# Optimization experiments

Measured on AMD Instinct MI355X. Metric: run time of the kernel, lower is better.

Reference implementation:

```python
import jax, jax.numpy as jnp
import numpy as np

N, K, DN, DA, H = 20000, 16, 128, 128, 256
D_IN = DN + DA  # 256


def _lin_init(key, out_dim, in_dim):
    scale = 1.0 / np.sqrt(in_dim)
    return jax.random.uniform(key, (out_dim, in_dim), jnp.float32, -scale, scale)


def setup_inputs() -> dict:
    key = jax.random.key(0)
    ks = jax.random.split(key, 16)
    # adjacency: col 0 = parent index; cols 1..K = neighbor indices, -1 padded.
    parent = jax.random.randint(ks[0], (N, 1), 0, N, dtype=jnp.int32)
    nbr_first = jax.random.randint(ks[1], (N, 1), 0, N, dtype=jnp.int32)  # guarantee >=1 nbr
    nbr_rest = jax.random.randint(ks[2], (N, K - 1), -1, N, dtype=jnp.int32)
    adj = jnp.concatenate([parent, nbr_first, nbr_rest], axis=1)
    names = jax.random.normal(ks[3], (N, DN), jnp.float32)
    attrs = jax.random.normal(ks[4], (N, DA), jnp.float32)
    return {
        "nodeAdjacencySpecTensor": adj,
        "nodeNamesEncoded": names,
        "nodeAttributesEncoded": attrs,
        "W_in": _lin_init(ks[5], H, D_IN),
        "b_in": jnp.zeros((H,), jnp.float32),
        "W_parent": _lin_init(ks[6], H, H),
        "b_parent": jnp.zeros((H,), jnp.float32),
        "W_neighbor": _lin_init(ks[7], H, H),
        "b_neighbor": jnp.zeros((H,), jnp.float32),
        "W_ih": _lin_init(ks[8], 3 * H, H),
        "b_ih": jnp.zeros((3 * H,), jnp.float32),
        "W_hh": _lin_init(ks[9], 3 * H, H),
        "b_hh": jnp.zeros((3 * H,), jnp.float32),
        "depth": 3,
    }


def _gru_cell(x, h, W_ih, b_ih, W_hh, b_hh):
    # torch.nn.GRUCell math; gate order r, z, n.
    gi = x @ W_ih.T + b_ih
    gh = h @ W_hh.T + b_hh
    i_r, i_z, i_n = jnp.split(gi, 3, axis=-1)
    h_r, h_z, h_n = jnp.split(gh, 3, axis=-1)
    r = jax.nn.sigmoid(i_r + h_r)
    z = jax.nn.sigmoid(i_z + h_z)
    n = jnp.tanh(i_n + r * h_n)
    return (1.0 - z) * n + z * h


def reference(nodeAdjacencySpecTensor, nodeNamesEncoded, nodeAttributesEncoded,
              W_in, b_in, W_parent, b_parent, W_neighbor, b_neighbor,
              W_ih, b_ih, W_hh, b_hh, depth):
    adj = nodeAdjacencySpecTensor
    parent_idx = adj[:, 0]                 # [N]
    nbr_idx = adj[:, 1:]                   # [N, K], -1 padded
    mask = (nbr_idx >= 0)                  # [N, K]
    safe_nbr = jnp.clip(nbr_idx, 0, None)
    nbr_count = jnp.maximum(mask.sum(axis=1), 1).astype(jnp.float32)  # [N]

    node_info = jnp.concatenate([nodeNamesEncoded, nodeAttributesEncoded], axis=-1)
    x = node_info @ W_in.T + b_in          # [N, H]

    for _ in range(depth):
        p = x @ W_parent.T + b_parent      # [N, H]
        nbr = x @ W_neighbor.T + b_neighbor  # [N, H]
        # irregular gathers
        parent_feat = p[parent_idx]        # [N, H]
        gathered = nbr[safe_nbr]           # [N, K, H]
        nbr_sum = jnp.sum(gathered * mask[:, :, None], axis=1)  # [N, H]
        summary = parent_feat + nbr_sum / nbr_count[:, None]
        x = _gru_cell(x, summary, W_ih, b_ih, W_hh, b_hh)
    return x
```

## Files before the change

### kernel.cpp

```cpp
#include <hip/hip_runtime.h>
#include <hip/hip_bf16.h>

typedef __bf16 bf16x8 __attribute__((ext_vector_type(8)));
typedef __bf16 bf16x4 __attribute__((ext_vector_type(4)));
typedef float  f32x4  __attribute__((ext_vector_type(4)));

#define NN   20000
#define NADJ 17

__device__ __forceinline__ void xcd_remap(int b, int nwg, int col_shift, int& r, int& c)
{
    int q = nwg >> 3, rem = nwg & 7;
    int x = b & 7, k = b >> 3;
    int start = x * q + (x < rem ? x : rem);
    int idx = start + k;
    r = idx >> col_shift;
    c = idx & ((1 << col_shift) - 1);
}

__global__ void pack_weights_kernel(const float* __restrict__ Win, const float* __restrict__ bin,
                                    const float* __restrict__ Wp,  const float* __restrict__ bp,
                                    const float* __restrict__ Wn,  const float* __restrict__ bn,
                                    const float* __restrict__ Wih, const float* __restrict__ bih,
                                    const float* __restrict__ Whh, const float* __restrict__ bhh,
                                    __bf16* __restrict__ Wb, float* __restrict__ bc)
{
    int idx = blockIdx.x * 256 + threadIdx.x;
    if (idx < 1536) {
        int c = idx; float v;
        if (c < 256)      v = bin[c];
        else if (c < 512) { int j = c - 256; v = bp[j] + bn[j]; }
        else {
            int rel = c - 512;
            int j = (rel >> 6) * 16 + (rel & 15);
            int g = (rel >> 4) & 3;
            if      (g == 0) v = bih[j] + bhh[j];
            else if (g == 1) v = bih[256 + j] + bhh[256 + j];
            else if (g == 2) v = bih[512 + j];
            else             v = bhh[512 + j];
        }
        bc[c] = v;
    }
    if (idx >= 180224) return;
    int e = idx << 2;
    const float* src = nullptr;
    bool zero = false;
    if (e < 65536) {
        int row = e >> 8, k = e & 255;
        src = Win + (size_t)row * 256 + k;
    } else if (e < 196608) {
        int rel = e - 65536;
        int row = rel >> 9, k = rel & 511;
        src = (k < 256) ? (Wp + (size_t)row * 256 + k)
                        : (Wn + (size_t)row * 256 + (k - 256));
    } else {
        int rel = e - 196608;
        int row = rel >> 9, k = rel & 511;
        int j = (row >> 6) * 16 + (row & 15);
        int g = (row >> 4) & 3;
        if (k < 256) {
            if (g == 3) zero = true;
            else {
                int off = (g == 0) ? 0 : (g == 1) ? 256 : 512;
                src = Wih + (size_t)(off + j) * 256 + k;
            }
        } else {
            int k2 = k - 256;
            if (g == 2) zero = true;
            else {
                int off = (g == 0) ? 0 : (g == 1) ? 256 : 512;
                src = Whh + (size_t)(off + j) * 256 + k2;
            }
        }
    }
    float4 v = zero ? make_float4(0.f, 0.f, 0.f, 0.f) : *(const float4*)src;
    bf16x4 o = { (__bf16)v.x, (__bf16)v.y, (__bf16)v.z, (__bf16)v.w };
    *(bf16x4*)(Wb + (size_t)e) = o;
}

__global__ void pack_info_kernel(const float* __restrict__ names, const float* __restrict__ attrs,
                                 __bf16* __restrict__ xb)
{
    int idx = blockIdx.x * 256 + threadIdx.x;
    if (idx >= NN * 64) return;
    int i  = idx >> 6;
    int d4 = (idx & 63) << 2;
    const float* src = (d4 < 128) ? (names + (size_t)i * 128 + d4)
                                  : (attrs + (size_t)i * 128 + (d4 - 128));
    float4 v = *(const float4*)src;
    bf16x4 o = { (__bf16)v.x, (__bf16)v.y, (__bf16)v.z, (__bf16)v.w };
    *(bf16x4*)(xb + (size_t)i * 256 + d4) = o;
}

__global__ void gather_avg_kernel(const int* __restrict__ adj, const __bf16* __restrict__ x,
                                  __bf16* __restrict__ G2)
{
    const int node = blockIdx.x * 4 + (threadIdx.x >> 6);
    const int l = threadIdx.x & 63;
    int av = (l < NADJ) ? adj[(size_t)node * NADJ + l] : -1;
    float s0 = 0.f, s1 = 0.f, s2 = 0.f, s3 = 0.f;
    int cnt = 0;
#pragma unroll
    for (int j = 1; j < NADJ; ++j) {
        int idx = __shfl(av, j, 64);
        if (idx >= 0) {
            ++cnt;
            bf16x4 v = *(const bf16x4*)(x + (size_t)idx * 256 + l * 4);
            s0 += (float)v[0]; s1 += (float)v[1]; s2 += (float)v[2]; s3 += (float)v[3];
        }
    }
    float inv = 1.f / (float)(cnt < 1 ? 1 : cnt);
    bf16x4 o = { (__bf16)(s0 * inv), (__bf16)(s1 * inv), (__bf16)(s2 * inv), (__bf16)(s3 * inv) };
    *(bf16x4*)(G2 + (size_t)node * 256 + l * 4) = o;
}

__global__ __launch_bounds__(256, 4)
void gemm_bias_kernel(const __bf16* __restrict__ A0, const __bf16* __restrict__ A1, int lda,
                      const int* __restrict__ parents, int par_stride,
                      const __bf16* __restrict__ W, int ldw,
                      const float* __restrict__ bias,
                      __bf16* __restrict__ Cb, __bf16* __restrict__ Cl,
                      int n_rows, int n_cols, int kt_n, int nwg, int col_shift)
{
    __shared__ __align__(16) __bf16 As[128 * 64];
    __shared__ __align__(16) __bf16 Bs[128 * 64];
    __shared__ int par_s[128];
    const int t = threadIdx.x;
    const int w = t >> 6;
    const int l = t & 63;
    int rb, cb_;
    xcd_remap(blockIdx.x, nwg, col_shift, rb, cb_);
    const int brow = rb * 128;
    const int bcol = cb_ * 128;
    const int wr = (w >> 1) * 64, wc = (w & 1) * 64;

    if (parents) {
        if (t < 128) {
            int node = brow + t; if (node > n_rows - 1) node = n_rows - 1;
            par_s[t] = parents[(size_t)node * par_stride];
        }
        __syncthreads();
    }

    f32x4 acc[4][4] = {};

    for (int kt = 0; kt < kt_n; ++kt) {
        const int k0 = kt * 64;
#pragma unroll
        for (int i = 0; i < 4; ++i) {
            int f   = i * 256 + t;
            int row = f >> 3;
            int cs  = ((f & 7) * 16) ^ ((row & 7) << 4);
            int ar  = brow + row; if (ar > n_rows - 1) ar = n_rows - 1;
            const __bf16* abase;
            if (parents && k0 < 256)             abase = A0 + (size_t)par_s[row] * 256 + k0;
            else if (A1 != nullptr && k0 >= 256) abase = A1 + (size_t)ar * 256 + (k0 - 256);
            else                                 abase = A0 + (size_t)ar * lda + k0;
            const __bf16* ga = abase + (cs >> 1);
            const __bf16* gb = W + (size_t)(bcol + row) * ldw + k0 + (cs >> 1);
            char* la = (char*)As + (i * 256 + w * 64) * 16;
            char* lb = (char*)Bs + (i * 256 + w * 64) * 16;
            __builtin_amdgcn_global_load_lds(
                (const __attribute__((address_space(1))) unsigned int*)ga,
                (__attribute__((address_space(3))) unsigned int*)la, 16, 0, 0);
            __builtin_amdgcn_global_load_lds(
                (const __attribute__((address_space(1))) unsigned int*)gb,
                (__attribute__((address_space(3))) unsigned int*)lb, 16, 0, 0);
        }
        asm volatile("s_waitcnt vmcnt(0)" ::: "memory");
        __syncthreads();
#pragma unroll
        for (int ks = 0; ks < 2; ++ks) {
            bf16x8 af[4], bfv[4];
#pragma unroll
            for (int m = 0; m < 4; ++m) {
                int row = wr + m * 16 + (l & 15);
                int cb  = (ks * 64 + ((l >> 4) * 16)) ^ ((row & 7) << 4);
                af[m] = *(const bf16x8*)((const char*)As + row * 128 + cb);
            }
#pragma unroll
            for (int n = 0; n < 4; ++n) {
                int row = wc + n * 16 + (l & 15);
                int cb  = (ks * 64 + ((l >> 4) * 16)) ^ ((row & 7) << 4);
                bfv[n] = *(const bf16x8*)((const char*)Bs + row * 128 + cb);
            }
#pragma unroll
            for (int m = 0; m < 4; ++m)
#pragma unroll
                for (int n = 0; n < 4; ++n)
                    acc[m][n] = __builtin_amdgcn_mfma_f32_16x16x32_bf16(af[m], bfv[n], acc[m][n], 0, 0, 0);
        }
        __syncthreads();
    }
#pragma unroll
    for (int m = 0; m < 4; ++m) {
        int r0 = brow + wr + m * 16 + ((l >> 4) * 4);
#pragma unroll
        for (int n = 0; n < 4; ++n) {
            int c = bcol + wc + n * 16 + (l & 15);
            float bv = bias[c];
#pragma unroll
            for (int i = 0; i < 4; ++i) {
                int r = r0 + i;
                if (r < n_rows) {
                    float v = acc[m][n][i] + bv;
                    __bf16 hi = (__bf16)v;
                    Cb[(size_t)r * n_cols + c] = hi;
                    if (Cl) Cl[(size_t)r * n_cols + c] = (__bf16)(v - (float)hi);
                }
            }
        }
    }
}

#define GRU_KT_BODY(K0, ABASE, SKIP_N)                                                  \
    {                                                                                   \
        _Pragma("unroll")                                                               \
        for (int i = 0; i < 4; ++i) {                                                   \
            int f   = i * 256 + t;                                                      \
            int row = f >> 3;                                                           \
            int cs  = ((f & 7) * 16) ^ ((row & 7) << 4);                                \
            int ar  = brow + row; if (ar > n_rows - 1) ar = n_rows - 1;                 \
            const __bf16* ga = (ABASE) + (size_t)ar * 256 + (cs >> 1);                  \
            const __bf16* gb = W + (size_t)(bcol + row) * 512 + (K0) + (cs >> 1);       \
            char* la = (char*)As + (i * 256 + w * 64) * 16;                             \
            char* lb = (char*)Bs + (i * 256 + w * 64) * 16;                             \
            __builtin_amdgcn_global_load_lds(                                           \
                (const __attribute__((address_space(1))) unsigned int*)ga,              \
                (__attribute__((address_space(3))) unsigned int*)la, 16, 0, 0);         \
            if (((row >> 4) & 3) != (SKIP_N))                                           \
                __builtin_amdgcn_global_load_lds(                                       \
                    (const __attribute__((address_space(1))) unsigned int*)gb,          \
                    (__attribute__((address_space(3))) unsigned int*)lb, 16, 0, 0);     \
        }                                                                               \
        asm volatile("s_waitcnt vmcnt(0)" ::: "memory");                                \
        __syncthreads();                                                                \
        _Pragma("unroll")                                                               \
        for (int ks = 0; ks < 2; ++ks) {                                                \
            bf16x8 af[4], bfv[4];                                                       \
            _Pragma("unroll")                                                           \
            for (int m = 0; m < 4; ++m) {                                               \
                int row = wr + m * 16 + (l & 15);                                       \
                int cb  = (ks * 64 + ((l >> 4) * 16)) ^ ((row & 7) << 4);               \
                af[m] = *(const bf16x8*)((const char*)As + row * 128 + cb);             \
            }                                                                           \
            _Pragma("unroll")                                                           \
            for (int n = 0; n < 4; ++n) {                                               \
                if (n == (SKIP_N)) continue;                                            \
                int row = wc + n * 16 + (l & 15);                                       \
                int cb  = (ks * 64 + ((l >> 4) * 16)) ^ ((row & 7) << 4);               \
                bfv[n] = *(const bf16x8*)((const char*)Bs + row * 128 + cb);            \
            }                                                                           \
            _Pragma("unroll")                                                           \
            for (int m = 0; m < 4; ++m)                                                 \
                _Pragma("unroll")                                                       \
                for (int n = 0; n < 4; ++n)                                             \
                    if (n != (SKIP_N))                                                  \
                        acc[m][n] = __builtin_amdgcn_mfma_f32_16x16x32_bf16(            \
                            af[m], bfv[n], acc[m][n], 0, 0, 0);                         \
        }                                                                               \
        __syncthreads();                                                                \
    }

__global__ __launch_bounds__(256, 4)
void gru_gemm_kernel(const __bf16* __restrict__ A0, const __bf16* __restrict__ A1,
                     const __bf16* __restrict__ W,
                     const float* __restrict__ bias,
                     const __bf16* __restrict__ sbh, const __bf16* __restrict__ sbl,
                     float* __restrict__ X, __bf16* __restrict__ xb_next,
                     int n_rows)
{
    __shared__ __align__(16) __bf16 As[128 * 64];
    __shared__ __align__(16) __bf16 Bs[128 * 64];
    const int t = threadIdx.x;
    const int w = t >> 6;
    const int l = t & 63;
    int rb, cb_;
    xcd_remap(blockIdx.x, 157 * 8, 3, rb, cb_);
    const int brow = rb * 128;
    const int bcol = cb_ * 128;
    const int wr = (w >> 1) * 64, wc = (w & 1) * 64;

    f32x4 acc[4][4] = {};

    for (int kt = 0; kt < 4; ++kt) {
        const int k0 = kt * 64;
        GRU_KT_BODY(k0, A0 + k0, 3)
    }
    for (int kt = 4; kt < 8; ++kt) {
        const int k0 = kt * 64;
        GRU_KT_BODY(k0, A1 + (k0 - 256), 2)
    }

    const int jb = ((bcol + wc) >> 6) * 16 + (l & 15);
    const int c0 = bcol + wc + (l & 15);
    const float b0 = bias[c0], b1 = bias[c0 + 16], b2 = bias[c0 + 32], b3 = bias[c0 + 48];
#pragma unroll
    for (int m = 0; m < 4; ++m) {
        int r0 = brow + wr + m * 16 + ((l >> 4) * 4);
#pragma unroll
        for (int i = 0; i < 4; ++i) {
            int r = r0 + i;
            if (r < n_rows) {
                float gr  = acc[m][0][i] + b0;
                float gz  = acc[m][1][i] + b1;
                float gin = acc[m][2][i] + b2;
                float ghn = acc[m][3][i] + b3;
                float rg = 1.f / (1.f + __expf(-gr));
                float zg = 1.f / (1.f + __expf(-gz));
                float a2 = gin + rg * ghn;
                float tt = __expf(-2.f * fabsf(a2));
                float ng = (1.f - tt) / (1.f + tt);
                ng = (a2 < 0.f) ? -ng : ng;
                float h = (float)sbh[(size_t)r * 256 + jb] + (float)sbl[(size_t)r * 256 + jb];
                float out = (1.f - zg) * ng + zg * h;
                if (X)       X[(size_t)r * 256 + jb] = out;
                if (xb_next) xb_next[(size_t)r * 256 + jb] = (__bf16)out;
            }
        }
    }
}

extern "C" void kernel_launch(void* const* d_in, const int* in_sizes, int n_in,
                              void* d_out, int out_size, void* d_ws, size_t ws_size,
                              hipStream_t stream)
{
    const int*   adj   = (const int*)  d_in[0];
    const float* names = (const float*)d_in[1];
    const float* attrs = (const float*)d_in[2];
    const float* Win = (const float*)d_in[3];
    const float* bin = (const float*)d_in[4];
    const float* Wp  = (const float*)d_in[5];
    const float* bp  = (const float*)d_in[6];
    const float* Wn  = (const float*)d_in[7];
    const float* bn  = (const float*)d_in[8];
    const float* Wih = (const float*)d_in[9];
    const float* bih = (const float*)d_in[10];
    const float* Whh = (const float*)d_in[11];
    const float* bhh = (const float*)d_in[12];
    float* X = (float*)d_out;

    char* w = (char*)d_ws;
    __bf16* xinfo = (__bf16*)(w);
    __bf16* xb0   = (__bf16*)(w + 10240000);
    __bf16* xb1   = (__bf16*)(w + 20480000);
    __bf16* sbh   = (__bf16*)(w + 30720000);
    __bf16* sbl   = (__bf16*)(w + 40960000);
    __bf16* G2    = (__bf16*)(w + 51200000);
    __bf16* Wb    = (__bf16*)(w + 61440000);
    float*  bc    = (float*) (w + 62881792);

    pack_weights_kernel<<<704, 256, 0, stream>>>(Win, bin, Wp, bp, Wn, bn, Wih, bih, Whh, bhh, Wb, bc);
    pack_info_kernel<<<5000, 256, 0, stream>>>(names, attrs, xinfo);

    gemm_bias_kernel<<<314, 256, 0, stream>>>(xinfo, nullptr, 256, nullptr, 0,
                                              Wb, 256, bc, xb0, nullptr, NN, 256, 4, 314, 1);

    __bf16* cur = xb0;
    __bf16* nxt = xb1;
    for (int d = 0; d < 3; ++d) {
        gather_avg_kernel<<<5000, 256, 0, stream>>>(adj, cur, G2);
        gemm_bias_kernel<<<314, 256, 0, stream>>>(cur, G2, 256, adj, NADJ,
                                                  Wb + 65536, 512, bc + 256,
                                                  sbh, sbl, NN, 256, 8, 314, 1);
        gru_gemm_kernel<<<1256, 256, 0, stream>>>(cur, sbh, Wb + 196608, bc + 512,
                                                  sbh, sbl, (d == 2) ? X : nullptr,
                                                  (d < 2) ? nxt : nullptr, NN);
        __bf16* tmp = cur; cur = nxt; nxt = tmp;
    }
}
```

Baseline: 259.0 us.

## Double-buffer LDS tiles to overlap global loads with MFMA in both GEMMs

Both the bias GEMM and the GRU GEMM now keep two LDS buffers for the A and B tiles. The loads for the next K tile are issued before the MFMAs run on the current one, and there is one barrier per iteration instead of two. The aim is to hide global-to-LDS load latency behind compute. In exchange, LDS use per block doubles and launch bounds drop from 4 to 2 blocks per CU. The explicit vmcnt(0) wait is removed, so visibility of the async LDS loads now depends on the wait the compiler emits at __syncthreads.

Result: slower. 281.8 us (+8.8%).

```diff
diff --git a/kernel.cpp b/kernel.cpp
--- a/kernel.cpp
+++ b/kernel.cpp
@@ -114,7 +114,7 @@
     *(bf16x4*)(G2 + (size_t)node * 256 + l * 4) = o;
 }
 
-__global__ __launch_bounds__(256, 4)
+__global__ __launch_bounds__(256, 2)
 void gemm_bias_kernel(const __bf16* __restrict__ A0, const __bf16* __restrict__ A1, int lda,
                       const int* __restrict__ parents, int par_stride,
                       const __bf16* __restrict__ W, int ldw,
@@ -122,8 +122,8 @@
                       __bf16* __restrict__ Cb, __bf16* __restrict__ Cl,
                       int n_rows, int n_cols, int kt_n, int nwg, int col_shift)
 {
-    __shared__ __align__(16) __bf16 As[128 * 64];
-    __shared__ __align__(16) __bf16 Bs[128 * 64];
+    __shared__ __align__(16) __bf16 As[2][128 * 64];
+    __shared__ __align__(16) __bf16 Bs[2][128 * 64];
     __shared__ int par_s[128];
     const int t = threadIdx.x;
     const int w = t >> 6;
@@ -142,9 +142,7 @@
         __syncthreads();
     }
 
-    f32x4 acc[4][4] = {};
-
-    for (int kt = 0; kt < kt_n; ++kt) {
+    auto stage = [&](int kt, int buf) {
         const int k0 = kt * 64;
 #pragma unroll
         for (int i = 0; i < 4; ++i) {
@@ -158,8 +156,8 @@
             else                                 abase = A0 + (size_t)ar * lda + k0;
             const __bf16* ga = abase + (cs >> 1);
             const __bf16* gb = W + (size_t)(bcol + row) * ldw + k0 + (cs >> 1);
-            char* la = (char*)As + (i * 256 + w * 64) * 16;
-            char* lb = (char*)Bs + (i * 256 + w * 64) * 16;
+            char* la = (char*)As[buf] + (i * 256 + w * 64) * 16;
+            char* lb = (char*)Bs[buf] + (i * 256 + w * 64) * 16;
             __builtin_amdgcn_global_load_lds(
                 (const __attribute__((address_space(1))) unsigned int*)ga,
                 (__attribute__((address_space(3))) unsigned int*)la, 16, 0, 0);
@@ -167,8 +165,15 @@
                 (const __attribute__((address_space(1))) unsigned int*)gb,
                 (__attribute__((address_space(3))) unsigned int*)lb, 16, 0, 0);
         }
-        asm volatile("s_waitcnt vmcnt(0)" ::: "memory");
-        __syncthreads();
+    };
+
+    f32x4 acc[4][4] = {};
+    stage(0, 0);
+    __syncthreads();
+
+    for (int kt = 0; kt < kt_n; ++kt) {
+        const int buf = kt & 1;
+        if (kt + 1 < kt_n) stage(kt + 1, buf ^ 1);
 #pragma unroll
         for (int ks = 0; ks < 2; ++ks) {
             bf16x8 af[4], bfv[4];
@@ -176,13 +181,13 @@
             for (int m = 0; m < 4; ++m) {
                 int row = wr + m * 16 + (l & 15);
                 int cb  = (ks * 64 + ((l >> 4) * 16)) ^ ((row & 7) << 4);
-                af[m] = *(const bf16x8*)((const char*)As + row * 128 + cb);
+                af[m] = *(const bf16x8*)((const char*)As[buf] + row * 128 + cb);
             }
 #pragma unroll
             for (int n = 0; n < 4; ++n) {
                 int row = wc + n * 16 + (l & 15);
                 int cb  = (ks * 64 + ((l >> 4) * 16)) ^ ((row & 7) << 4);
-                bfv[n] = *(const bf16x8*)((const char*)Bs + row * 128 + cb);
+                bfv[n] = *(const bf16x8*)((const char*)Bs[buf] + row * 128 + cb);
             }
 #pragma unroll
             for (int m = 0; m < 4; ++m)
@@ -190,7 +195,7 @@
                 for (int n = 0; n < 4; ++n)
                     acc[m][n] = __builtin_amdgcn_mfma_f32_16x16x32_bf16(af[m], bfv[n], acc[m][n], 0, 0, 0);
         }
-        __syncthreads();
+        if (kt + 1 < kt_n) __syncthreads();
     }
 #pragma unroll
     for (int m = 0; m < 4; ++m) {
@@ -213,28 +218,33 @@
     }
 }
 
-#define GRU_KT_BODY(K0, ABASE, SKIP_N)                                                  \
+#define GRU_STAGE(KN, BUF)                                                              \
     {                                                                                   \
+        const int k0_   = (KN) * 64;                                                    \
+        const int skip_ = ((KN) < 4) ? 3 : 2;                                           \
+        const __bf16* ab_ = ((KN) < 4) ? (A0 + k0_) : (A1 + (k0_ - 256));               \
         _Pragma("unroll")                                                               \
         for (int i = 0; i < 4; ++i) {                                                   \
             int f   = i * 256 + t;                                                      \
             int row = f >> 3;                                                           \
             int cs  = ((f & 7) * 16) ^ ((row & 7) << 4);                                \
             int ar  = brow + row; if (ar > n_rows - 1) ar = n_rows - 1;                 \
-            const __bf16* ga = (ABASE) + (size_t)ar * 256 + (cs >> 1);                  \
-            const __bf16* gb = W + (size_t)(bcol + row) * 512 + (K0) + (cs >> 1);       \
-            char* la = (char*)As + (i * 256 + w * 64) * 16;                             \
-            char* lb = (char*)Bs + (i * 256 + w * 64) * 16;                             \
+            const __bf16* ga = ab_ + (size_t)ar * 256 + (cs >> 1);                      \
+            const __bf16* gb = W + (size_t)(bcol + row) * 512 + k0_ + (cs >> 1);        \
+            char* la = (char*)As[BUF] + (i * 256 + w * 64) * 16;                        \
+            char* lb = (char*)Bs[BUF] + (i * 256 + w * 64) * 16;                        \
             __builtin_amdgcn_global_load_lds(                                           \
                 (const __attribute__((address_space(1))) unsigned int*)ga,              \
                 (__attribute__((address_space(3))) unsigned int*)la, 16, 0, 0);         \
-            if (((row >> 4) & 3) != (SKIP_N))                                           \
+            if (((row >> 4) & 3) != skip_)                                              \
                 __builtin_amdgcn_global_load_lds(                                       \
                     (const __attribute__((address_space(1))) unsigned int*)gb,          \
                     (__attribute__((address_space(3))) unsigned int*)lb, 16, 0, 0);     \
         }                                                                               \
-        asm volatile("s_waitcnt vmcnt(0)" ::: "memory");                                \
-        __syncthreads();                                                                \
+    }
+
+#define GRU_COMPUTE(BUF, SKIPN)                                                         \
+    {                                                                                   \
         _Pragma("unroll")                                                               \
         for (int ks = 0; ks < 2; ++ks) {                                                \
             bf16x8 af[4], bfv[4];                                                       \
@@ -242,27 +252,26 @@
             for (int m = 0; m < 4; ++m) {                                               \
                 int row = wr + m * 16 + (l & 15);                                       \
                 int cb  = (ks * 64 + ((l >> 4) * 16)) ^ ((row & 7) << 4);               \
-                af[m] = *(const bf16x8*)((const char*)As + row * 128 + cb);             \
+                af[m] = *(const bf16x8*)((const char*)As[BUF] + row * 128 + cb);        \
             }                                                                           \
             _Pragma("unroll")                                                           \
             for (int n = 0; n < 4; ++n) {                                               \
-                if (n == (SKIP_N)) continue;                                            \
+                if (n == (SKIPN)) continue;                                             \
                 int row = wc + n * 16 + (l & 15);                                       \
                 int cb  = (ks * 64 + ((l >> 4) * 16)) ^ ((row & 7) << 4);               \
-                bfv[n] = *(const bf16x8*)((const char*)Bs + row * 128 + cb);            \
+                bfv[n] = *(const bf16x8*)((const char*)Bs[BUF] + row * 128 + cb);       \
             }                                                                           \
             _Pragma("unroll")                                                           \
             for (int m = 0; m < 4; ++m)                                                 \
                 _Pragma("unroll")                                                       \
                 for (int n = 0; n < 4; ++n)                                             \
-                    if (n != (SKIP_N))                                                  \
+                    if (n != (SKIPN))                                                   \
                         acc[m][n] = __builtin_amdgcn_mfma_f32_16x16x32_bf16(            \
                             af[m], bfv[n], acc[m][n], 0, 0, 0);                         \
         }                                                                               \
-        __syncthreads();                                                                \
-    }
-
-__global__ __launch_bounds__(256, 4)
+    }
+
+__global__ __launch_bounds__(256, 2)
 void gru_gemm_kernel(const __bf16* __restrict__ A0, const __bf16* __restrict__ A1,
                      const __bf16* __restrict__ W,
                      const float* __restrict__ bias,
@@ -270,8 +279,8 @@
                      float* __restrict__ X, __bf16* __restrict__ xb_next,
                      int n_rows)
 {
-    __shared__ __align__(16) __bf16 As[128 * 64];
-    __shared__ __align__(16) __bf16 Bs[128 * 64];
+    __shared__ __align__(16) __bf16 As[2][128 * 64];
+    __shared__ __align__(16) __bf16 Bs[2][128 * 64];
     const int t = threadIdx.x;
     const int w = t >> 6;
     const int l = t & 63;
@@ -283,13 +292,15 @@
 
     f32x4 acc[4][4] = {};
 
-    for (int kt = 0; kt < 4; ++kt) {
-        const int k0 = kt * 64;
-        GRU_KT_BODY(k0, A0 + k0, 3)
-    }
-    for (int kt = 4; kt < 8; ++kt) {
-        const int k0 = kt * 64;
-        GRU_KT_BODY(k0, A1 + (k0 - 256), 2)
+    GRU_STAGE(0, 0)
+    __syncthreads();
+#pragma unroll
+    for (int kt = 0; kt < 8; ++kt) {
+        const int buf = kt & 1;
+        if (kt < 7) { GRU_STAGE(kt + 1, buf ^ 1) }
+        const int skipn = (kt < 4) ? 3 : 2;
+        GRU_COMPUTE(buf, skipn)
+        if (kt < 7) __syncthreads();
     }
 
     const int jb = ((bcol + wc) >> 6) * 16 + (l & 15);
```
